# Kernel tuning notes

Measured on AMD Instinct MI355X. Metric: run time of the kernel, lower is better.

The kernel has to match this reference:

```python
import jax, jax.numpy as jnp
import numpy as np

B, N, D = 16, 512, 768
H, E = 12, 8
HD = D // H


def setup_inputs() -> dict:
    key = jax.random.key(0)
    ks = jax.random.split(key, 10)
    s = 0.02
    return {
        "x": jax.random.normal(ks[0], (B, N, D), jnp.float32),
        "gating_weights": jax.random.uniform(ks[1], (B, E), jnp.float32),
        "Wq": jax.random.normal(ks[2], (E, D, D), jnp.float32) * s,
        "bq": jax.random.normal(ks[3], (E, D), jnp.float32) * s,
        "Wk": jax.random.normal(ks[4], (E, D, D), jnp.float32) * s,
        "bk": jax.random.normal(ks[5], (E, D), jnp.float32) * s,
        "Wv": jax.random.normal(ks[6], (E, D, D), jnp.float32) * s,
        "bv": jax.random.normal(ks[7], (E, D), jnp.float32) * s,
        "Wo": jax.random.normal(ks[8], (D, D), jnp.float32) * s,
        "bo": jax.random.normal(ks[9], (D,), jnp.float32) * s,
    }


def _gated_proj(x, g, W, b):
    # sum_e g[b,e] * (x @ W_e.T + b_e)  ==  x @ (sum_e g[b,e] W_e).T + sum_e g[b,e] b_e
    # W: [E, out, in] (torch Linear layout). Fold gating into per-sample weight.
    Wc = jnp.einsum('be,eoi->boi', g, W)      # [B, out, in]
    bc = jnp.einsum('be,eo->bo', g, b)        # [B, out]
    return jnp.einsum('bni,boi->bno', x, Wc) + bc[:, None, :]


def reference(x, gating_weights, Wq, bq, Wk, bk, Wv, bv, Wo, bo):
    g = gating_weights
    Q = _gated_proj(x, g, Wq, bq)  # [B, N, D]
    K = _gated_proj(x, g, Wk, bk)
    V = _gated_proj(x, g, Wv, bv)
    Q = Q.reshape(B, N, H, HD).transpose(0, 2, 1, 3)  # [B, H, N, HD]
    K = K.reshape(B, N, H, HD).transpose(0, 2, 1, 3)
    V = V.reshape(B, N, H, HD).transpose(0, 2, 1, 3)
    scores = jnp.einsum('bhnd,bhmd->bhnm', Q, K) / jnp.sqrt(jnp.float32(HD))
    attn = jax.nn.softmax(scores, axis=-1)            # [B, H, N, N]
    ctx = jnp.einsum('bhnm,bhmd->bhnd', attn, V)
    ctx = ctx.transpose(0, 2, 1, 3).reshape(B, N, D)
    out = jnp.einsum('bnd,od->bno', ctx, Wo) + bo
    return (out, attn)
```

## Files before the change

### kernel.cpp

```cpp
#include <hip/hip_runtime.h>
#include <hip/hip_bf16.h>

#define Bc 16
#define Nc 512
#define Dc 768
#define Hc 12
#define Ec 8
#define HDc 64
#define D3 (3 * Dc)
#define ZS ((size_t)Bc * Hc * Nc * HDc)

#define NBW  (Dc * Dc / 4 / 256)
#define NBB  (Bc * Dc / 256)
#define NBWO (Dc * Dc / 8 / 256)
#define NBX  (Bc * Nc * Dc / 8 / 256)

typedef __hip_bfloat16 bf16;
typedef short bf16x8 __attribute__((ext_vector_type(8)));
typedef float f32x4 __attribute__((ext_vector_type(4)));
typedef unsigned short u16x4 __attribute__((ext_vector_type(4)));

__device__ __forceinline__ unsigned int f2bf(float f) {
    union { __hip_bfloat16 h; unsigned short u; } cv;
    cv.h = __float2bfloat16(f);
    return (unsigned int)cv.u;
}

__device__ __forceinline__ void gload16(const void* src, void* ldsDst) {
    __builtin_amdgcn_global_load_lds((const __attribute__((address_space(1))) void*)src,
                                     (__attribute__((address_space(3))) void*)ldsDst,
                                     16, 0, 0);
}

__global__ __launch_bounds__(256) void prep_kernel(const float* __restrict__ g,
                                                   const float* __restrict__ W0,
                                                   const float* __restrict__ W1,
                                                   const float* __restrict__ W2,
                                                   const float* __restrict__ b0,
                                                   const float* __restrict__ b1,
                                                   const float* __restrict__ b2,
                                                   const float* __restrict__ Wo,
                                                   const float* __restrict__ x,
                                                   bf16* __restrict__ Wc,
                                                   float* __restrict__ bc,
                                                   bf16* __restrict__ Wo_bf,
                                                   bf16* __restrict__ x_bf) {
    __shared__ float gs[Bc * Ec];
    int blk = blockIdx.x, tid = threadIdx.x;
    if (blk < 3 * NBW) {
        if (tid < Bc * Ec) gs[tid] = g[tid];
        __syncthreads();
        int t = blk / NBW;
        const float* W = (t == 0) ? W0 : ((t == 1) ? W1 : W2);
        int p = (blk - t * NBW) * 256 + tid;
        f32x4 w[Ec];
#pragma unroll
        for (int e = 0; e < Ec; ++e) w[e] = ((const f32x4*)W)[(size_t)e * (Dc * Dc / 4) + p];
        int o = p / (Dc / 4), i4 = p - o * (Dc / 4);
#pragma unroll
        for (int b = 0; b < Bc; ++b) {
            f32x4 acc = {0.f, 0.f, 0.f, 0.f};
#pragma unroll
            for (int e = 0; e < Ec; ++e) {
                float ge = gs[b * Ec + e];
                acc[0] += ge * w[e][0]; acc[1] += ge * w[e][1];
                acc[2] += ge * w[e][2]; acc[3] += ge * w[e][3];
            }
            u16x4 ov;
#pragma unroll
            for (int j = 0; j < 4; ++j) ov[j] = (unsigned short)f2bf(acc[j]);
            *(u16x4*)&Wc[((size_t)b * D3 + t * Dc + o) * Dc + i4 * 4] = ov;
        }
    } else if (blk < 3 * NBW + NBB) {
        int i = (blk - 3 * NBW) * 256 + tid;
        int b = i / Dc, o = i - b * Dc;
        const float* bs[3] = {b0, b1, b2};
#pragma unroll
        for (int t = 0; t < 3; ++t) {
            float acc = 0.f;
#pragma unroll
            for (int e = 0; e < Ec; ++e) acc += g[b * Ec + e] * bs[t][e * Dc + o];
            bc[(size_t)b * D3 + t * Dc + o] = acc;
        }
    } else if (blk < 3 * NBW + NBB + NBWO) {
        int i = (blk - 3 * NBW - NBB) * 256 + tid;
        f32x4 a = ((const f32x4*)Wo)[i * 2];
        f32x4 b = ((const f32x4*)Wo)[i * 2 + 1];
        unsigned short t[8];
#pragma unroll
        for (int j = 0; j < 4; ++j) { t[j] = (unsigned short)f2bf(a[j]); t[4 + j] = (unsigned short)f2bf(b[j]); }
        ((bf16x8*)Wo_bf)[i] = *(bf16x8*)t;
    } else {
        int i = (blk - 3 * NBW - NBB - NBWO) * 256 + tid;
        f32x4 a = ((const f32x4*)x)[i * 2];
        f32x4 b = ((const f32x4*)x)[i * 2 + 1];
        unsigned short t[8];
#pragma unroll
        for (int j = 0; j < 4; ++j) { t[j] = (unsigned short)f2bf(a[j]); t[4 + j] = (unsigned short)f2bf(b[j]); }
        ((bf16x8*)x_bf)[i] = *(bf16x8*)t;
    }
}

template<int BM, int BN, int OMODE, int NBN, int NBM>
__global__ __launch_bounds__(256) void gemm_mfma(const bf16* __restrict__ Ain,
                                                 const bf16* __restrict__ Bin,
                                                 void* __restrict__ Cout,
                                                 const float* __restrict__ bias,
                                                 int lda, int ldb, int ldc, int K,
                                                 long sA, long sB, long sC, int sBias) {
    constexpr int A_LDS = BM * 128;
    constexpr int B_LDS = BN * 128;
    __shared__ __align__(16) char lds[A_LDS + B_LDS];
    char* ldsA = lds;
    char* ldsB = lds + A_LDS;

    const int tid = threadIdx.x;
    const int lane = tid & 63;
    const int wave = tid >> 6;
    const int wr = wave >> 1, wc = wave & 1;
    constexpr int TM = BM / 32;
    constexpr int TN = BN / 32;

    constexpr int PERZ = NBN * NBM;
    int L = blockIdx.x;
    int xcd = L & 7, i = L >> 3;
    int zi = (i >= PERZ) ? 1 : 0;
    const int z = xcd * 2 + zi;
    int j = i - zi * PERZ;
    const int n0 = (j % NBN) * BN;
    const int m0 = (j / NBN) * BM;

    const int mbase = wr * (BM / 2);
    const int nbase = wc * (BN / 2);

    const bf16* Ab = Ain + (size_t)z * sA;
    const bf16* Bb = Bin + (size_t)z * sB;

    f32x4 acc[TM][TN];
#pragma unroll
    for (int m = 0; m < TM; ++m)
#pragma unroll
        for (int n = 0; n < TN; ++n) acc[m][n] = f32x4{0.f, 0.f, 0.f, 0.f};

    constexpr int ACH = BM / 64;
    constexpr int BCH = BN / 64;

    for (int k0 = 0; k0 < K; k0 += 64) {
#pragma unroll
        for (int hh = 0; hh < 2; ++hh)
#pragma unroll
            for (int c = 0; c < ACH; ++c) {
                int q = wave * ACH + c;
                int row = q * 16 + (lane >> 2);
                int sl = (lane & 3) ^ (row & 3);
                const bf16* src = Ab + (size_t)(m0 + row) * lda + k0 + hh * 32 + sl * 8;
                gload16(src, ldsA + hh * (BM * 64) + q * 1024);
            }
#pragma unroll
        for (int hh = 0; hh < 2; ++hh)
#pragma unroll
            for (int c = 0; c < BCH; ++c) {
                int q = wave * BCH + c;
                int row = q * 16 + (lane >> 2);
                int sl = (lane & 3) ^ (row & 3);
                const bf16* src = Bb + (size_t)(n0 + row) * ldb + k0 + hh * 32 + sl * 8;
                gload16(src, ldsB + hh * (BN * 64) + q * 1024);
            }
        __syncthreads();

#pragma unroll
        for (int hh = 0; hh < 2; ++hh) {
            bf16x8 af[TM], bfr[TN];
#pragma unroll
            for (int m = 0; m < TM; ++m) {
                int r = mbase + m * 16 + (lane & 15);
                int sp = (lane >> 4) ^ (lane & 3);
                af[m] = *(const bf16x8*)(ldsA + hh * (BM * 64) + r * 64 + sp * 16);
            }
#pragma unroll
            for (int n = 0; n < TN; ++n) {
                int r = nbase + n * 16 + (lane & 15);
                int sp = (lane >> 4) ^ (lane & 3);
                bfr[n] = *(const bf16x8*)(ldsB + hh * (BN * 64) + r * 64 + sp * 16);
            }
#pragma unroll
            for (int m = 0; m < TM; ++m)
#pragma unroll
                for (int n = 0; n < TN; ++n)
                    acc[m][n] = __builtin_amdgcn_mfma_f32_16x16x32_bf16(af[m], bfr[n], acc[m][n], 0, 0, 0);
        }
        __syncthreads();
    }

#pragma unroll
    for (int n = 0; n < TN; ++n) {
        int colbase = n0 + nbase + n * 16;
        int col = colbase + (lane & 15);
        float bv = bias ? bias[(size_t)z * sBias + col] : 0.f;
        if constexpr (OMODE == 1) {
            int t = colbase / Dc;
            int within = colbase - t * Dc;
            int h = within >> 6;
            int dbase = within & 63;
            if (t == 2) {
                bf16* vp = (bf16*)Cout + 2 * ZS
                         + (((size_t)(z * Hc + h) * 16) * 4 + (dbase >> 4)) * 512
                         + (size_t)lane * 8;
#pragma unroll
                for (int m = 0; m < TM; ++m) {
                    int rowblk = m0 + mbase + m * 16;
                    int c = rowblk >> 5, jb = (rowblk >> 4) & 1;
                    uint2 wv = {f2bf(acc[m][n][0] + bv) | (f2bf(acc[m][n][1] + bv) << 16),
                                f2bf(acc[m][n][2] + bv) | (f2bf(acc[m][n][3] + bv) << 16)};
                    *(uint2*)(vp + (size_t)c * 2048 + jb * 4) = wv;
                }
            } else {
                float qs = (t == 0) ? 0.125f : 1.0f;
                bf16* dst = (bf16*)Cout + (size_t)t * ZS
                          + ((size_t)(z * Hc + h) * Nc) * HDc + dbase + (lane & 15);
#pragma unroll
                for (int m = 0; m < TM; ++m) {
                    int row = m0 + mbase + m * 16 + (lane >> 4) * 4;
#pragma unroll
                    for (int r = 0; r < 4; ++r)
                        dst[(size_t)(row + r) * HDc] = __float2bfloat16((acc[m][n][r] + bv) * qs);
                }
            }
        } else {
            size_t cOff = (size_t)z * sC;
#pragma unroll
            for (int m = 0; m < TM; ++m) {
                int row = m0 + mbase + m * 16 + (lane >> 4) * 4;
#pragma unroll
                for (int r = 0; r < 4; ++r)
                    __builtin_nontemporal_store(acc[m][n][r] + bv,
                        &((float*)Cout)[cOff + (size_t)(row + r) * ldc + col]);
            }
        }
    }
}

__global__ __launch_bounds__(256) void fused_attn_kernel(const bf16* __restrict__ Qz,
                                                         const bf16* __restrict__ Kz,
                                                         const bf16* __restrict__ Vp,
                                                         float* __restrict__ attn,
                                                         bf16* __restrict__ ctx) {
    __shared__ float msum[2][2][4][16];
    __shared__ __align__(16) char plds[2][16][1024];

    int L = blockIdx.x;
    int z = (L & 7) + 8 * (L >> 7);
    int qt = (L >> 3) & 15;
    int b = z / Hc, h = z - b * Hc;
    int wave = threadIdx.x >> 6, lane = threadIdx.x & 63;
    int cl = lane & 15, hi = lane >> 4;
    int qbase = qt * 32;

    const bf16* Qb = Qz + (size_t)z * Nc * HDc;
    bf16x8 qf[2][2];
#pragma unroll
    for (int t = 0; t < 2; ++t) {
        const bf16* qrow = Qb + (size_t)(qbase + t * 16 + cl) * HDc + hi * 8;
        qf[t][0] = *(const bf16x8*)(qrow);
        qf[t][1] = *(const bf16x8*)(qrow + 32);
    }

    const bf16* Kb = Kz + ((size_t)z * Nc + wave * 128) * HDc;
    f32x4 s0[8], s1[8];
#pragma unroll
    for (int n = 0; n < 8; ++n) {
        const bf16* krow = Kb + (n * 16 + cl) * HDc + hi * 8;
        bf16x8 k0 = *(const bf16x8*)(krow);
        bf16x8 k1 = *(const bf16x8*)(krow + 32);
        f32x4 a0 = {0.f, 0.f, 0.f, 0.f};
        a0 = __builtin_amdgcn_mfma_f32_16x16x32_bf16(k0, qf[0][0], a0, 0, 0, 0);
        a0 = __builtin_amdgcn_mfma_f32_16x16x32_bf16(k1, qf[0][1], a0, 0, 0, 0);
        s0[n] = a0;
        f32x4 a1 = {0.f, 0.f, 0.f, 0.f};
        a1 = __builtin_amdgcn_mfma_f32_16x16x32_bf16(k0, qf[1][0], a1, 0, 0, 0);
        a1 = __builtin_amdgcn_mfma_f32_16x16x32_bf16(k1, qf[1][1], a1, 0, 0, 0);
        s1[n] = a1;
    }

    f32x4 mx0 = s0[0], mx1 = s1[0];
#pragma unroll
    for (int n = 1; n < 8; ++n)
#pragma unroll
        for (int r = 0; r < 4; ++r) {
            mx0[r] = fmaxf(mx0[r], s0[n][r]);
            mx1[r] = fmaxf(mx1[r], s1[n][r]);
        }
    float mw0 = fmaxf(fmaxf(mx0[0], mx0[1]), fmaxf(mx0[2], mx0[3]));
    float mw1 = fmaxf(fmaxf(mx1[0], mx1[1]), fmaxf(mx1[2], mx1[3]));
    mw0 = fmaxf(mw0, __shfl_xor(mw0, 16)); mw0 = fmaxf(mw0, __shfl_xor(mw0, 32));
    mw1 = fmaxf(mw1, __shfl_xor(mw1, 16)); mw1 = fmaxf(mw1, __shfl_xor(mw1, 32));

    f32x4 sa0 = {0.f, 0.f, 0.f, 0.f}, sa1 = {0.f, 0.f, 0.f, 0.f};
#pragma unroll
    for (int n = 0; n < 8; ++n)
#pragma unroll
        for (int r = 0; r < 4; ++r) {
            float e0 = __expf(s0[n][r] - mw0); s0[n][r] = e0; sa0[r] += e0;
            float e1 = __expf(s1[n][r] - mw1); s1[n][r] = e1; sa1[r] += e1;
        }
    float sw0 = (sa0[0] + sa0[1]) + (sa0[2] + sa0[3]);
    float sw1 = (sa1[0] + sa1[1]) + (sa1[2] + sa1[3]);
    sw0 += __shfl_xor(sw0, 16); sw0 += __shfl_xor(sw0, 32);
    sw1 += __shfl_xor(sw1, 16); sw1 += __shfl_xor(sw1, 32);
    if (lane < 16) {
        msum[0][0][wave][cl] = mw0; msum[0][1][wave][cl] = mw1;
        msum[1][0][wave][cl] = sw0; msum[1][1][wave][cl] = sw1;
    }

    char* prow0 = plds[0][cl];
    char* prow1 = plds[1][cl];
    int swz = (cl & 7) << 4;
#pragma unroll
    for (int n = 0; n < 8; ++n) {
        int off = ((wave * 4 + (n >> 1)) * 64 + hi * 16 + (n & 1) * 8) ^ swz;
        uint2 w0v = {f2bf(s0[n][0]) | (f2bf(s0[n][1]) << 16),
                     f2bf(s0[n][2]) | (f2bf(s0[n][3]) << 16)};
        uint2 w1v = {f2bf(s1[n][0]) | (f2bf(s1[n][1]) << 16),
                     f2bf(s1[n][2]) | (f2bf(s1[n][3]) << 16)};
        *(uint2*)(prow0 + off) = w0v;
        *(uint2*)(prow1 + off) = w1v;
    }

    const bf16* Vb = Vp + (size_t)z * 16 * 4 * 512;
    bf16x8 vpre[8];
#pragma unroll
    for (int c = 0; c < 8; ++c)
        vpre[c] = *(const bf16x8*)(Vb + ((c * 4 + wave) * 64 + lane) * 8);

    __syncthreads();

    float m0 = fmaxf(fmaxf(msum[0][0][0][cl], msum[0][0][1][cl]),
                     fmaxf(msum[0][0][2][cl], msum[0][0][3][cl]));
    float m1 = fmaxf(fmaxf(msum[0][1][0][cl], msum[0][1][1][cl]),
                     fmaxf(msum[0][1][2][cl], msum[0][1][3][cl]));
    float a00 = __expf(msum[0][0][0][cl] - m0), a01 = __expf(msum[0][0][1][cl] - m0);
    float a02 = __expf(msum[0][0][2][cl] - m0), a03 = __expf(msum[0][0][3][cl] - m0);
    float a10 = __expf(msum[0][1][0][cl] - m1), a11 = __expf(msum[0][1][1][cl] - m1);
    float a12 = __expf(msum[0][1][2][cl] - m1), a13 = __expf(msum[0][1][3][cl] - m1);
    float inv0 = 1.0f / (msum[1][0][0][cl] * a00 + msum[1][0][1][cl] * a01 +
                         msum[1][0][2][cl] * a02 + msum[1][0][3][cl] * a03);
    float inv1 = 1.0f / (msum[1][1][0][cl] * a10 + msum[1][1][1][cl] * a11 +
                         msum[1][1][2][cl] * a12 + msum[1][1][3][cl] * a13);

    float mw0g = __expf(mw0 - m0) * inv0;
    float mw1g = __expf(mw1 - m1) * inv1;
    float* arow0 = attn + (size_t)z * Nc * Nc + (size_t)(qbase + cl) * Nc + wave * 128;
    float* arow1 = arow0 + 16 * Nc;
#pragma unroll
    for (int n = 0; n < 8; ++n) {
        f32x4 p0, p1;
#pragma unroll
        for (int r = 0; r < 4; ++r) { p0[r] = s0[n][r] * mw0g; p1[r] = s1[n][r] * mw1g; }
        __builtin_nontemporal_store(p0, (f32x4*)(arow0 + n * 16 + hi * 4));
        __builtin_nontemporal_store(p1, (f32x4*)(arow1 + n * 16 + hi * 4));
    }

    f32x4 o0a[4], o1a[4];
#pragma unroll
    for (int w = 0; w < 4; ++w) { o0a[w] = f32x4{0.f, 0.f, 0.f, 0.f}; o1a[w] = f32x4{0.f, 0.f, 0.f, 0.f}; }
#pragma unroll
    for (int c = 0; c < 16; ++c) {
        bf16x8 vf = (c < 8) ? vpre[c]
                            : *(const bf16x8*)(Vb + ((c * 4 + wave) * 64 + lane) * 8);
        bf16x8 pf0 = *(const bf16x8*)(prow0 + ((c * 64 + hi * 16) ^ swz));
        bf16x8 pf1 = *(const bf16x8*)(prow1 + ((c * 64 + hi * 16) ^ swz));
        o0a[c >> 2] = __builtin_amdgcn_mfma_f32_16x16x32_bf16(vf, pf0, o0a[c >> 2], 0, 0, 0);
        o1a[c >> 2] = __builtin_amdgcn_mfma_f32_16x16x32_bf16(vf, pf1, o1a[c >> 2], 0, 0, 0);
    }
    f32x4 o0 = o0a[0] * a00 + o0a[1] * a01 + o0a[2] * a02 + o0a[3] * a03;
    f32x4 o1 = o1a[0] * a10 + o1a[1] * a11 + o1a[2] * a12 + o1a[3] * a13;

    bf16* cb0 = ctx + ((size_t)b * Nc + qbase + cl) * Dc + h * HDc + wave * 16;
    bf16* cb1 = cb0 + (size_t)16 * Dc;
    uint2 wv0 = {f2bf(o0[0] * inv0) | (f2bf(o0[1] * inv0) << 16),
                 f2bf(o0[2] * inv0) | (f2bf(o0[3] * inv0) << 16)};
    uint2 wv1 = {f2bf(o1[0] * inv1) | (f2bf(o1[1] * inv1) << 16),
                 f2bf(o1[2] * inv1) | (f2bf(o1[3] * inv1) << 16)};
    *(uint2*)(cb0 + hi * 4) = wv0;
    *(uint2*)(cb1 + hi * 4) = wv1;
}

extern "C" void kernel_launch(void* const* d_in, const int* in_sizes, int n_in,
                              void* d_out, int out_size, void* d_ws, size_t ws_size,
                              hipStream_t stream) {
    (void)in_sizes; (void)n_in; (void)out_size; (void)ws_size;
    const float* x  = (const float*)d_in[0];
    const float* g  = (const float*)d_in[1];
    const float* Wq = (const float*)d_in[2];
    const float* bq = (const float*)d_in[3];
    const float* Wk = (const float*)d_in[4];
    const float* bk = (const float*)d_in[5];
    const float* Wv = (const float*)d_in[6];
    const float* bv = (const float*)d_in[7];
    const float* Wo = (const float*)d_in[8];
    const float* bo = (const float*)d_in[9];

    float* out  = (float*)d_out;
    float* attn = out + (size_t)Bc * Nc * Dc;

    char* w = (char*)d_ws;
    bf16* x_bf  = (bf16*)w;
    bf16* Wo_bf = x_bf + (size_t)Bc * Nc * Dc;
    float* bc   = (float*)(Wo_bf + (size_t)Dc * Dc);
    bf16* Qz    = (bf16*)(bc + (size_t)Bc * D3);
    bf16* Kz    = Qz + ZS;
    bf16* Vp    = Qz + 2 * ZS;
    bf16* Wc    = Vp + ZS;
    bf16* ctx   = Wc;

    dim3 blk(256);

    prep_kernel<<<dim3(3 * NBW + NBB + NBWO + NBX), blk, 0, stream>>>(
        g, Wq, Wk, Wv, bq, bk, bv, Wo, x, Wc, bc, Wo_bf, x_bf);

    gemm_mfma<128, 192, 1, 12, 4><<<dim3(768), blk, 0, stream>>>(
        x_bf, Wc, Qz, bc, Dc, Dc, 0, Dc,
        (long)Nc * Dc, (long)D3 * Dc, 0L, D3);

    fused_attn_kernel<<<dim3(Bc * Hc * (Nc / 32)), blk, 0, stream>>>(Qz, Kz, Vp, attn, ctx);

    gemm_mfma<64, 128, 0, 6, 8><<<dim3(768), blk, 0, stream>>>(
        ctx, Wo_bf, out, bo, Dc, Dc, Dc, Dc,
        (long)Nc * Dc, 0L, (long)Nc * Dc, 0);
}
```

Measured before the change: 172.4 us.

## Double-buffer LDS tiles in MFMA GEMM to overlap global loads with compute

Result: no change. 173.3 us (+0.5%).

```diff
diff --git a/kernel.cpp b/kernel.cpp
--- a/kernel.cpp
+++ b/kernel.cpp
@@ -108,11 +108,8 @@
                                                  const float* __restrict__ bias,
                                                  int lda, int ldb, int ldc, int K,
                                                  long sA, long sB, long sC, int sBias) {
-    constexpr int A_LDS = BM * 128;
-    constexpr int B_LDS = BN * 128;
-    __shared__ __align__(16) char lds[A_LDS + B_LDS];
-    char* ldsA = lds;
-    char* ldsB = lds + A_LDS;
+    constexpr int HALF = (BM + BN) * 64;
+    __shared__ __align__(16) char lds[2 * HALF];
 
     const int tid = threadIdx.x;
     const int lane = tid & 63;
@@ -145,52 +142,56 @@
     constexpr int ACH = BM / 64;
     constexpr int BCH = BN / 64;
 
-    for (int k0 = 0; k0 < K; k0 += 64) {
-#pragma unroll
-        for (int hh = 0; hh < 2; ++hh)
-#pragma unroll
-            for (int c = 0; c < ACH; ++c) {
-                int q = wave * ACH + c;
-                int row = q * 16 + (lane >> 2);
-                int sl = (lane & 3) ^ (row & 3);
-                const bf16* src = Ab + (size_t)(m0 + row) * lda + k0 + hh * 32 + sl * 8;
-                gload16(src, ldsA + hh * (BM * 64) + q * 1024);
-            }
-#pragma unroll
-        for (int hh = 0; hh < 2; ++hh)
-#pragma unroll
-            for (int c = 0; c < BCH; ++c) {
-                int q = wave * BCH + c;
-                int row = q * 16 + (lane >> 2);
-                int sl = (lane & 3) ^ (row & 3);
-                const bf16* src = Bb + (size_t)(n0 + row) * ldb + k0 + hh * 32 + sl * 8;
-                gload16(src, ldsB + hh * (BN * 64) + q * 1024);
-            }
+    auto stage = [&](int sel, int k0) {
+        char* base = lds + sel * HALF;
+#pragma unroll
+        for (int c = 0; c < ACH; ++c) {
+            int q = wave * ACH + c;
+            int row = q * 16 + (lane >> 2);
+            int sl = (lane & 3) ^ (row & 3);
+            gload16(Ab + (size_t)(m0 + row) * lda + k0 + sl * 8, base + q * 1024);
+        }
+#pragma unroll
+        for (int c = 0; c < BCH; ++c) {
+            int q = wave * BCH + c;
+            int row = q * 16 + (lane >> 2);
+            int sl = (lane & 3) ^ (row & 3);
+            gload16(Bb + (size_t)(n0 + row) * ldb + k0 + sl * 8, base + BM * 64 + q * 1024);
+        }
+    };
+
+    auto compute = [&](int sel) {
+        char* base = lds + sel * HALF;
+        bf16x8 af[TM], bfr[TN];
+#pragma unroll
+        for (int m = 0; m < TM; ++m) {
+            int r = mbase + m * 16 + (lane & 15);
+            int sp = (lane >> 4) ^ (lane & 3);
+            af[m] = *(const bf16x8*)(base + r * 64 + sp * 16);
+        }
+#pragma unroll
+        for (int n = 0; n < TN; ++n) {
+            int r = nbase + n * 16 + (lane & 15);
+            int sp = (lane >> 4) ^ (lane & 3);
+            bfr[n] = *(const bf16x8*)(base + BM * 64 + r * 64 + sp * 16);
+        }
+#pragma unroll
+        for (int m = 0; m < TM; ++m)
+#pragma unroll
+            for (int n = 0; n < TN; ++n)
+                acc[m][n] = __builtin_amdgcn_mfma_f32_16x16x32_bf16(af[m], bfr[n], acc[m][n], 0, 0, 0);
+    };
+
+    stage(0, 0);
+    __syncthreads();
+    int cur = 0;
+    for (int k0 = 32; k0 < K; k0 += 32) {
+        stage(cur ^ 1, k0);
+        compute(cur);
         __syncthreads();
-
-#pragma unroll
-        for (int hh = 0; hh < 2; ++hh) {
-            bf16x8 af[TM], bfr[TN];
-#pragma unroll
-            for (int m = 0; m < TM; ++m) {
-                int r = mbase + m * 16 + (lane & 15);
-                int sp = (lane >> 4) ^ (lane & 3);
-                af[m] = *(const bf16x8*)(ldsA + hh * (BM * 64) + r * 64 + sp * 16);
-            }
-#pragma unroll
-            for (int n = 0; n < TN; ++n) {
-                int r = nbase + n * 16 + (lane & 15);
-                int sp = (lane >> 4) ^ (lane & 3);
-                bfr[n] = *(const bf16x8*)(ldsB + hh * (BN * 64) + r * 64 + sp * 16);
-            }
-#pragma unroll
-            for (int m = 0; m < TM; ++m)
-#pragma unroll
-                for (int n = 0; n < TN; ++n)
-                    acc[m][n] = __builtin_amdgcn_mfma_f32_16x16x32_bf16(af[m], bfr[n], acc[m][n], 0, 0, 0);
-        }
-        __syncthreads();
-    }
+        cur ^= 1;
+    }
+    compute(cur);
 
 #pragma unroll
     for (int n = 0; n < TN; ++n) {
```
